# Performance work log

Hardware: AMD Instinct MI355X
Metric: run time of the kernel (lower is better)

Reference implementation:

```python
import jax, jax.numpy as jnp
import numpy as np


def setup_inputs() -> dict:
    key = jax.random.key(0)
    k1, k2, k3 = jax.random.split(key, 3)
    B, C, H, W = 2, 32, 128, 256
    maxdisp = 12
    feat_l = jax.random.normal(k1, (B, C, H, W), dtype=jnp.float32)
    feat_r = jax.random.normal(k2, (B, C, H, W), dtype=jnp.float32)
    # disparity estimate in pixels at this feature scale
    disp = jax.random.uniform(k3, (B, 1, H, W), dtype=jnp.float32) * 64.0
    return {"feat_l": feat_l, "feat_r": feat_r, "disp": disp, "maxdisp": maxdisp}


def _warp_1d(feat_r, d_map):
    """Warp feat_r [B,C,H,W] horizontally by d_map [B,H,W].

    Equivalent to torch grid_sample(bilinear, zeros padding, align_corners=True)
    with grid x = xx - d, y = yy: y lands exactly on pixel centers, so the
    bilinear interp degenerates to 1-D interp along W with zero padding.
    """
    B, C, H, W = feat_r.shape
    xx = jnp.arange(W, dtype=feat_r.dtype)
    px = xx[None, None, :] - d_map  # [B,H,W] sampling x-coordinate
    x0 = jnp.floor(px)
    w1 = px - x0                     # weight of right neighbor
    w0 = 1.0 - w1
    x0i = x0.astype(jnp.int32)
    x1i = x0i + 1
    m0 = ((x0i >= 0) & (x0i <= W - 1)).astype(feat_r.dtype)  # zeros padding
    m1 = ((x1i >= 0) & (x1i <= W - 1)).astype(feat_r.dtype)

    def gather(idx):
        idxc = jnp.clip(idx, 0, W - 1)[:, None, :, :]  # [B,1,H,W]
        return jnp.take_along_axis(feat_r, jnp.broadcast_to(idxc, (B, C, H, W)), axis=3)

    g0 = gather(x0i)
    g1 = gather(x1i)
    return g0 * (w0 * m0)[:, None] + g1 * (w1 * m1)[:, None]  # [B,C,H,W]


def reference(feat_l, feat_r, disp, maxdisp):
    B, C, H, W = feat_l.shape
    D = 2 * maxdisp - 1
    shifts = jnp.arange(-maxdisp + 1, maxdisp, dtype=feat_l.dtype)  # [D]
    # batch_disp - batch_shift, laid out [D,B,H,W] (plane-major for vmap)
    d_all = disp[:, 0][None, :, :, :] - shifts[:, None, None, None]  # [D,B,H,W]
    warped = jax.vmap(lambda d: _warp_1d(feat_r, d))(d_all)          # [D,B,C,H,W]
    # L1 norm over channels of (feat_l - warped)
    cost = jnp.sum(jnp.abs(feat_l[None] - warped), axis=2)           # [D,B,H,W]
    return jnp.transpose(cost, (1, 0, 2, 3))                         # [B,D,H,W]
```

## Files before the change

kernel.cpp:

```cpp
#include <hip/hip_runtime.h>

#define BB 2
#define CC 32
#define HH 128
#define WW 256
#define DD 23
#define HW (HH * WW)

#define SEG 64
#define NSEG 4
#define NCOLS 151
#define SC 36
#define RED 23


__global__ __launch_bounds__(256, 4) void cost_volume_kernel(
    const float* __restrict__ feat_l,
    const float* __restrict__ feat_r,
    const float* __restrict__ disp,
    float* __restrict__ out)
{
    __shared__ __align__(16) float smem[NCOLS * SC];

    const int t  = threadIdx.x;
    const int q  = t >> 6;
    const int px = t & 63;
    const int s  = blockIdx.x >> 8;
    const int bh = blockIdx.x & 255;
    const int b  = bh >> 7;
    const int h  = bh & 127;
    const int w  = s * SEG + px;
    const int COL0 = s * SEG - 75;
    const int c0 = q * 8;

    float fl[8];
    const size_t lbase = ((size_t)(b * CC + c0)) * HW + (size_t)h * WW + w;
    #pragma unroll
    for (int k = 0; k < 8; ++k) fl[k] = feat_l[lbase + (size_t)k * HW];
    const float d = disp[(size_t)bh * WW + w];

    #pragma unroll
    for (int cc = 0; cc < 3; ++cc) {
        const int col = cc * 64 + px;
        if (col < NCOLS) {
            const int  gcol = col + COL0;
            const bool inr  = (gcol >= 0) && (gcol < WW);
            const int  gc   = min(max(gcol, 0), WW - 1);
            #pragma unroll
            for (int qq = 0; qq < 2; ++qq) {
                const int cq = (q + 4 * qq) * 4;
                const size_t base = ((size_t)(b * CC + cq)) * HW + (size_t)h * WW + gc;
                const float x0 = feat_r[base];
                const float x1 = feat_r[base + HW];
                const float x2 = feat_r[base + 2 * HW];
                const float x3 = feat_r[base + 3 * HW];
                float4 v;
                v.x = inr ? x0 : 0.0f;
                v.y = inr ? x1 : 0.0f;
                v.z = inr ? x2 : 0.0f;
                v.w = inr ? x3 : 0.0f;
                *(float4*)&smem[col * SC + cq] = v;
            }
        }
    }
    __syncthreads();

    const float pxf = (float)w - d;
    const float x0f = floorf(pxf);
    const float w1  = pxf - x0f;
    const float w0  = 1.0f - w1;
    int lb = (int)x0f - COL0 - 11;
    lb = min(max(lb, 0), NCOLS - 24);

    float4 Ta[3], Tb[3];
    #define LOADTAP(idx, j) { \
        const float4* p_ = (const float4*)&smem[(lb + (j)) * SC + c0]; \
        Ta[idx] = p_[0]; Tb[idx] = p_[1]; }

    LOADTAP(0, 0)
    LOADTAP(1, 1)

    float acc[DD];
    #pragma unroll
    for (int di = 0; di < DD; ++di) {
        if (di + 2 < 24) LOADTAP((di + 2) % 3, di + 2)
        const float4 A0 = Ta[di % 3],       A1 = Tb[di % 3];
        const float4 B0 = Ta[(di + 1) % 3], B1 = Tb[(di + 1) % 3];
        float sA = 0.0f, sB = 0.0f;
        sA += fabsf(fmaf(w0, A0.x, fmaf(w1, B0.x, -fl[0])));
        sB += fabsf(fmaf(w0, A0.y, fmaf(w1, B0.y, -fl[1])));
        sA += fabsf(fmaf(w0, A0.z, fmaf(w1, B0.z, -fl[2])));
        sB += fabsf(fmaf(w0, A0.w, fmaf(w1, B0.w, -fl[3])));
        sA += fabsf(fmaf(w0, A1.x, fmaf(w1, B1.x, -fl[4])));
        sB += fabsf(fmaf(w0, A1.y, fmaf(w1, B1.y, -fl[5])));
        sA += fabsf(fmaf(w0, A1.z, fmaf(w1, B1.z, -fl[6])));
        sB += fabsf(fmaf(w0, A1.w, fmaf(w1, B1.w, -fl[7])));
        acc[di] = sA + sB;
    }
    #undef LOADTAP

    __syncthreads();
    if (q != 0) {
        float* r = &smem[(q - 1) * (64 * RED) + px * RED];
        #pragma unroll
        for (int di = 0; di < DD; ++di) r[di] = acc[di];
    }
    __syncthreads();
    if (q == 0) {
        const float* r0 = &smem[0 * (64 * RED) + px * RED];
        const float* r1 = &smem[1 * (64 * RED) + px * RED];
        const float* r2 = &smem[2 * (64 * RED) + px * RED];
        #pragma unroll
        for (int di = 0; di < DD; ++di) {
            const float v = acc[di] + r0[di] + r1[di] + r2[di];
            out[((size_t)(b * DD + di)) * HW + (size_t)h * WW + w] = v;
        }
    }
}

extern "C" void kernel_launch(void* const* d_in, const int* in_sizes, int n_in,
                              void* d_out, int out_size, void* d_ws, size_t ws_size,
                              hipStream_t stream)
{
    const float* feat_l = (const float*)d_in[0];
    const float* feat_r = (const float*)d_in[1];
    const float* disp   = (const float*)d_in[2];
    float* out = (float*)d_out;

    dim3 grid(NSEG * BB * HH);
    dim3 block(256);
    cost_volume_kernel<<<grid, block, 0, stream>>>(feat_l, feat_r, disp, out);
}
```

Baseline: 78.01 us.

## Split channels across 8 wavegroups with 512-thread blocks and two-stage reduction

Doubles the block size so each thread handles 4 channels instead of 8, halving per-thread register and compute work across the 23 disparity taps. The cross-channel reduction becomes two-stage through shared memory, with enlarged LDS buffer. Aims to raise parallelism and latency hiding, at the cost of extra synchronization and reduction traffic.

Result: no change. 77.67 us (-0.4%).

```diff
diff --git a/kernel.cpp b/kernel.cpp
--- a/kernel.cpp
+++ b/kernel.cpp
@@ -11,16 +11,17 @@
 #define NSEG 4
 #define NCOLS 151
 #define SC 36
-#define RED 23
+#define SLAB (64 * DD)
+#define SMEMN 5888
 
 
-__global__ __launch_bounds__(256, 4) void cost_volume_kernel(
+__global__ __launch_bounds__(512, 8) void cost_volume_kernel(
     const float* __restrict__ feat_l,
     const float* __restrict__ feat_r,
     const float* __restrict__ disp,
     float* __restrict__ out)
 {
-    __shared__ __align__(16) float smem[NCOLS * SC];
+    __shared__ __align__(16) float smem[SMEMN];
 
     const int t  = threadIdx.x;
     const int q  = t >> 6;
@@ -31,12 +32,12 @@
     const int h  = bh & 127;
     const int w  = s * SEG + px;
     const int COL0 = s * SEG - 75;
-    const int c0 = q * 8;
+    const int c0 = q * 4;
 
-    float fl[8];
+    float fl[4];
     const size_t lbase = ((size_t)(b * CC + c0)) * HW + (size_t)h * WW + w;
     #pragma unroll
-    for (int k = 0; k < 8; ++k) fl[k] = feat_l[lbase + (size_t)k * HW];
+    for (int k = 0; k < 4; ++k) fl[k] = feat_l[lbase + (size_t)k * HW];
     const float d = disp[(size_t)bh * WW + w];
 
     #pragma unroll
@@ -46,21 +47,17 @@
             const int  gcol = col + COL0;
             const bool inr  = (gcol >= 0) && (gcol < WW);
             const int  gc   = min(max(gcol, 0), WW - 1);
-            #pragma unroll
-            for (int qq = 0; qq < 2; ++qq) {
-                const int cq = (q + 4 * qq) * 4;
-                const size_t base = ((size_t)(b * CC + cq)) * HW + (size_t)h * WW + gc;
-                const float x0 = feat_r[base];
-                const float x1 = feat_r[base + HW];
-                const float x2 = feat_r[base + 2 * HW];
-                const float x3 = feat_r[base + 3 * HW];
-                float4 v;
-                v.x = inr ? x0 : 0.0f;
-                v.y = inr ? x1 : 0.0f;
-                v.z = inr ? x2 : 0.0f;
-                v.w = inr ? x3 : 0.0f;
-                *(float4*)&smem[col * SC + cq] = v;
-            }
+            const size_t base = ((size_t)(b * CC + c0)) * HW + (size_t)h * WW + gc;
+            const float x0 = feat_r[base];
+            const float x1 = feat_r[base + HW];
+            const float x2 = feat_r[base + 2 * HW];
+            const float x3 = feat_r[base + 3 * HW];
+            float4 v;
+            v.x = inr ? x0 : 0.0f;
+            v.y = inr ? x1 : 0.0f;
+            v.z = inr ? x2 : 0.0f;
+            v.w = inr ? x3 : 0.0f;
+            *(float4*)&smem[col * SC + c0] = v;
         }
     }
     __syncthreads();
@@ -72,10 +69,9 @@
     int lb = (int)x0f - COL0 - 11;
     lb = min(max(lb, 0), NCOLS - 24);
 
-    float4 Ta[3], Tb[3];
-    #define LOADTAP(idx, j) { \
-        const float4* p_ = (const float4*)&smem[(lb + (j)) * SC + c0]; \
-        Ta[idx] = p_[0]; Tb[idx] = p_[1]; }
+    float4 T[3];
+    #define LOADTAP(idx, j) \
+        T[idx] = *(const float4*)&smem[(lb + (j)) * SC + c0];
 
     LOADTAP(0, 0)
     LOADTAP(1, 1)
@@ -84,32 +80,40 @@
     #pragma unroll
     for (int di = 0; di < DD; ++di) {
         if (di + 2 < 24) LOADTAP((di + 2) % 3, di + 2)
-        const float4 A0 = Ta[di % 3],       A1 = Tb[di % 3];
-        const float4 B0 = Ta[(di + 1) % 3], B1 = Tb[(di + 1) % 3];
-        float sA = 0.0f, sB = 0.0f;
-        sA += fabsf(fmaf(w0, A0.x, fmaf(w1, B0.x, -fl[0])));
-        sB += fabsf(fmaf(w0, A0.y, fmaf(w1, B0.y, -fl[1])));
-        sA += fabsf(fmaf(w0, A0.z, fmaf(w1, B0.z, -fl[2])));
-        sB += fabsf(fmaf(w0, A0.w, fmaf(w1, B0.w, -fl[3])));
-        sA += fabsf(fmaf(w0, A1.x, fmaf(w1, B1.x, -fl[4])));
-        sB += fabsf(fmaf(w0, A1.y, fmaf(w1, B1.y, -fl[5])));
-        sA += fabsf(fmaf(w0, A1.z, fmaf(w1, B1.z, -fl[6])));
-        sB += fabsf(fmaf(w0, A1.w, fmaf(w1, B1.w, -fl[7])));
+        const float4 A = T[di % 3];
+        const float4 Bv = T[(di + 1) % 3];
+        float sA, sB;
+        sA  = fabsf(fmaf(w0, A.x, fmaf(w1, Bv.x, -fl[0])));
+        sB  = fabsf(fmaf(w0, A.y, fmaf(w1, Bv.y, -fl[1])));
+        sA += fabsf(fmaf(w0, A.z, fmaf(w1, Bv.z, -fl[2])));
+        sB += fabsf(fmaf(w0, A.w, fmaf(w1, Bv.w, -fl[3])));
         acc[di] = sA + sB;
     }
     #undef LOADTAP
 
     __syncthreads();
-    if (q != 0) {
-        float* r = &smem[(q - 1) * (64 * RED) + px * RED];
+    if (q >= 4) {
+        float* r = &smem[(q - 4) * SLAB + px * DD];
+        #pragma unroll
+        for (int di = 0; di < DD; ++di) r[di] = acc[di];
+    }
+    __syncthreads();
+    if (q < 4) {
+        const float* r = &smem[q * SLAB + px * DD];
+        #pragma unroll
+        for (int di = 0; di < DD; ++di) acc[di] += r[di];
+    }
+    __syncthreads();
+    if (q >= 1 && q < 4) {
+        float* r = &smem[(q - 1) * SLAB + px * DD];
         #pragma unroll
         for (int di = 0; di < DD; ++di) r[di] = acc[di];
     }
     __syncthreads();
     if (q == 0) {
-        const float* r0 = &smem[0 * (64 * RED) + px * RED];
-        const float* r1 = &smem[1 * (64 * RED) + px * RED];
-        const float* r2 = &smem[2 * (64 * RED) + px * RED];
+        const float* r0 = &smem[0 * SLAB + px * DD];
+        const float* r1 = &smem[1 * SLAB + px * DD];
+        const float* r2 = &smem[2 * SLAB + px * DD];
         #pragma unroll
         for (int di = 0; di < DD; ++di) {
             const float v = acc[di] + r0[di] + r1[di] + r2[di];
@@ -128,6 +132,6 @@
     float* out = (float*)d_out;
 
     dim3 grid(NSEG * BB * HH);
-    dim3 block(256);
+    dim3 block(512);
     cost_volume_kernel<<<grid, block, 0, stream>>>(feat_l, feat_r, disp, out);
 }
```
